# Performance work log

Hardware: AMD Instinct MI355X
Metric: run time of the kernel (lower is better)

The kernel has to match this reference:

```python
import jax, jax.numpy as jnp
import numpy as np

N = 50000      # nodes
E = 640000     # edges
DIN = 256      # in_channels
DE = 64        # edge_dim
H1 = 128       # hidden_channels (conv1 out)
H2 = 64        # hidden_channels//2 (conv2 out)
OUT = 1


def tconv(x, src, dst, edge_attr, Wq, bq, Wk, bk, Wv, bv, We, Ws, bs):
    """PyG TransformerConv, heads=1, concat=True, root_weight=True."""
    n = x.shape[0]
    C = Wq.shape[1]
    q = x @ Wq + bq                      # [N, C]
    k = x @ Wk + bk                      # [N, C]
    v = x @ Wv + bv                      # [N, C]
    e = edge_attr @ We                   # [E, C] (lin_edge has no bias)
    k_e = k[src] + e                     # key_j + edge_emb per edge
    alpha = jnp.sum(q[dst] * k_e, axis=-1) / jnp.sqrt(jnp.float32(C))  # [E]
    # neighborhood softmax over incoming edges of each dst node
    m = jax.ops.segment_max(alpha, dst, num_segments=n)
    ex = jnp.exp(alpha - m[dst])
    denom = jax.ops.segment_sum(ex, dst, num_segments=n)
    a = ex / (denom[dst] + 1e-16)
    msg = a[:, None] * (v[src] + e)      # [E, C]
    out = jax.ops.segment_sum(msg, dst, num_segments=n)  # [N, C]
    return out + x @ Ws + bs             # root/skip connection


def setup_inputs() -> dict:
    key = jax.random.key(0)
    ks = jax.random.split(key, 24)
    p = lambda k, shape: jax.random.normal(k, shape, jnp.float32) * 0.02
    inp = {
        "x": jax.random.normal(ks[0], (N, DIN), jnp.float32),
        "edge_index": jax.random.randint(ks[1], (2, E), 0, N),
        "edge_attr": jax.random.normal(ks[2], (E, DE), jnp.float32),
        # conv1 params (in=DIN -> out=H1)
        "Wq1": p(ks[3], (DIN, H1)), "bq1": jnp.zeros((H1,), jnp.float32),
        "Wk1": p(ks[4], (DIN, H1)), "bk1": jnp.zeros((H1,), jnp.float32),
        "Wv1": p(ks[5], (DIN, H1)), "bv1": jnp.zeros((H1,), jnp.float32),
        "We1": p(ks[6], (DE, H1)),
        "Ws1": p(ks[7], (DIN, H1)), "bs1": jnp.zeros((H1,), jnp.float32),
        # conv2 params (in=H1 -> out=H2)
        "Wq2": p(ks[8], (H1, H2)), "bq2": jnp.zeros((H2,), jnp.float32),
        "Wk2": p(ks[9], (H1, H2)), "bk2": jnp.zeros((H2,), jnp.float32),
        "Wv2": p(ks[10], (H1, H2)), "bv2": jnp.zeros((H2,), jnp.float32),
        "We2": p(ks[11], (DE, H2)),
        "Ws2": p(ks[12], (H1, H2)), "bs2": jnp.zeros((H2,), jnp.float32),
        # classifier
        "Wc": p(ks[13], (H2, OUT)), "bc": jnp.zeros((OUT,), jnp.float32),
    }
    return inp


def reference(x, edge_index, edge_attr,
              Wq1, bq1, Wk1, bk1, Wv1, bv1, We1, Ws1, bs1,
              Wq2, bq2, Wk2, bk2, Wv2, bv2, We2, Ws2, bs2,
              Wc, bc):
    src, dst = edge_index[0], edge_index[1]
    h = tconv(x, src, dst, edge_attr, Wq1, bq1, Wk1, bk1, Wv1, bv1, We1, Ws1, bs1)
    h = jax.nn.relu(h)  # dropout is identity in eval mode
    h = tconv(h, src, dst, edge_attr, Wq2, bq2, Wk2, bk2, Wv2, bv2, We2, Ws2, bs2)
    h = jax.nn.relu(h)
    return h @ Wc + bc  # [N, 1] logits
```

## Files before the change

### kernel.cpp

```cpp
#include <hip/hip_runtime.h>
#include <math.h>

constexpr int NN  = 50000;
constexpr int NE  = 640000;
constexpr int DIN = 256;
constexpr int DE  = 64;
constexpr int H1  = 128;
constexpr int H2  = 64;
constexpr int EWS = H1 + H2;

using u16 = unsigned short;
typedef __attribute__((ext_vector_type(8))) short bf16x8;
typedef __attribute__((ext_vector_type(4))) float f32x4;

__device__ inline u16 f2bf(float f) {
  unsigned u = __float_as_uint(f);
  unsigned r = (u + 0x7FFFu + ((u >> 16) & 1u)) >> 16;
  return (u16)r;
}
__device__ inline float bf2f(u16 h) { return __uint_as_float(((unsigned)h) << 16); }
__device__ inline unsigned pack2(u16 a, u16 b) {
  return (unsigned)a | ((unsigned)b << 16);
}
__device__ inline f32x4 mfma16(bf16x8 a, bf16x8 b, f32x4 c) {
  return __builtin_amdgcn_mfma_f32_16x16x32_bf16(a, b, c, 0, 0, 0);
}

__global__ __launch_bounds__(256) void packwt_kernel(
    const float* __restrict__ W0, const float* __restrict__ W1,
    const float* __restrict__ W2, const float* __restrict__ W3,
    const float* __restrict__ b0, const float* __restrict__ b1,
    const float* __restrict__ b2, const float* __restrict__ b3,
    u16* __restrict__ Bth, u16* __restrict__ Btl, float* __restrict__ bcat,
    int K, int C, int nmats) {
  int total = nmats * C * K;
  for (int idx = blockIdx.x * blockDim.x + threadIdx.x; idx < total;
       idx += gridDim.x * blockDim.x) {
    int k = idx % K;
    int n = idx / K;
    int which = n / C, cc = n % C;
    const float* W = which == 0 ? W0 : which == 1 ? W1 : which == 2 ? W2 : W3;
    float v = W[k * C + cc];
    u16 h = f2bf(v);
    Bth[(size_t)n * K + k] = h;
    Btl[(size_t)n * K + k] = f2bf(v - bf2f(h));
    if (k == 0 && bcat) {
      const float* b = which == 0 ? b0 : which == 1 ? b1 : which == 2 ? b2 : b3;
      bcat[n] = b ? b[cc] : 0.f;
    }
  }
}

__global__ __launch_bounds__(256) void hist_kernel(const int* __restrict__ dst,
                                                   int* __restrict__ deg, int nE) {
  int e = blockIdx.x * blockDim.x + threadIdx.x;
  if (e < nE) atomicAdd(&deg[dst[e]], 1);
}

__global__ __launch_bounds__(256) void scan1_kernel(const int* __restrict__ deg,
                                                    int* __restrict__ part,
                                                    int* __restrict__ chunkSums,
                                                    int n) {
  __shared__ int s[256];
  int tid = threadIdx.x;
  int i = blockIdx.x * 256 + tid;
  int v0 = (i < n) ? deg[i] : 0;
  s[tid] = v0;
  __syncthreads();
  for (int off = 1; off < 256; off <<= 1) {
    int v = (tid >= off) ? s[tid - off] : 0;
    __syncthreads();
    s[tid] += v;
    __syncthreads();
  }
  if (i < n) part[i] = s[tid];
  if (tid == 255) chunkSums[blockIdx.x] = s[255];
}

__global__ __launch_bounds__(256) void scan2_kernel(int* __restrict__ chunkSums,
                                                    int nchunks) {
  __shared__ int s[256];
  int tid = threadIdx.x;
  s[tid] = (tid < nchunks) ? chunkSums[tid] : 0;
  __syncthreads();
  for (int off = 1; off < 256; off <<= 1) {
    int v = (tid >= off) ? s[tid - off] : 0;
    __syncthreads();
    s[tid] += v;
    __syncthreads();
  }
  if (tid < nchunks) chunkSums[tid] = s[tid];
}

__global__ __launch_bounds__(256) void scan3_kernel(const int* __restrict__ deg,
                                                    const int* __restrict__ part,
                                                    const int* __restrict__ chunkSums,
                                                    int* __restrict__ row_start,
                                                    int n, int nE) {
  int i = blockIdx.x * 256 + threadIdx.x;
  if (i < n)
    row_start[i] = part[i] - deg[i] + (blockIdx.x ? chunkSums[blockIdx.x - 1] : 0);
  if (i == 0) row_start[n] = nE;
}

__global__ __launch_bounds__(256) void scatter_kernel(const int* __restrict__ dst,
                                                      const int* __restrict__ row_start,
                                                      int* __restrict__ cursor,
                                                      int* __restrict__ eid, int nE) {
  int e = blockIdx.x * blockDim.x + threadIdx.x;
  if (e >= nE) return;
  int d = dst[e];
  int pos = row_start[d] + atomicAdd(&cursor[d], 1);
  eid[pos] = e;
}

__global__ __launch_bounds__(256) void sort_extract_kernel(
    int* __restrict__ eid, const int* __restrict__ row_start,
    const int* __restrict__ srcI, int* __restrict__ src_csr, int n) {
  int v = blockIdx.x * blockDim.x + threadIdx.x;
  if (v >= n) return;
  int b = row_start[v], e = row_start[v + 1];
  for (int i = b + 1; i < e; i++) {
    int key = eid[i];
    int j = i - 1;
    while (j >= b && eid[j] > key) { eid[j + 1] = eid[j]; j--; }
    eid[j + 1] = key;
  }
  for (int i = b; i < e; i++) src_csr[i] = srcI[eid[i]];
}

template <int BN, int EPI>
__global__ __launch_bounds__(256) void mfma_gemm_kernel(
    const float* __restrict__ A, const int* __restrict__ ridx,
    const u16* __restrict__ Bth, const u16* __restrict__ Btl,
    const float* __restrict__ bias, float* __restrict__ Cout,
    float* __restrict__ Qp, u16* __restrict__ KVp, float* __restrict__ Sp,
    int M, int Nn, int K, int Cl) {
  constexpr int BM = 128, BK = 32;
  constexpr int NI = BN / 32;
  constexpr int SM_STAGE = (BM + BN) * BK * 2;
  constexpr int SM_EPI = (EPI >= 1) ? BM * BN : 0;
  constexpr int SM = SM_STAGE > SM_EPI ? SM_STAGE : SM_EPI;
  __shared__ __align__(16) u16 smem[SM];
  u16* Ah = smem;
  u16* Al = smem + BM * BK;
  u16* Bh = smem + 2 * BM * BK;
  u16* Bl = smem + 2 * BM * BK + BN * BK;
  int tid = threadIdx.x;
  int lane = tid & 63, wid = tid >> 6;
  int wm = wid >> 1, wn = wid & 1;
  int row0 = blockIdx.y * BM, col0 = blockIdx.x * BN;
  int k8 = lane >> 4, rb = lane & 15;

  f32x4 acc[4][NI];
#pragma unroll
  for (int mi = 0; mi < 4; mi++)
#pragma unroll
    for (int ni = 0; ni < NI; ni++) acc[mi][ni] = (f32x4){0.f, 0.f, 0.f, 0.f};

  size_t aoff[2];
  int sdst[2];
  for (int p = 0; p < 2; p++) {
    int idx = p * 256 + tid;
    int r = idx >> 2, c = idx & 3;
    int ar = row0 + r;
    if (ar >= M) ar = M - 1;
    if (ridx) ar = ridx[ar];
    aoff[p] = (size_t)ar * K + c * 8;
    sdst[p] = r * BK + ((c ^ ((r >> 1) & 3)) << 3);
  }

  for (int k0 = 0; k0 < K; k0 += BK) {
    __syncthreads();
#pragma unroll
    for (int p = 0; p < 2; p++) {
      const float* s = A + aoff[p] + k0;
      float4 u = *(const float4*)s, v = *(const float4*)(s + 4);
      float f[8] = {u.x, u.y, u.z, u.w, v.x, v.y, v.z, v.w};
      u16 h[8], l[8];
#pragma unroll
      for (int j = 0; j < 8; j++) {
        h[j] = f2bf(f[j]);
        l[j] = f2bf(f[j] - bf2f(h[j]));
      }
      *(uint4*)&Ah[sdst[p]] = make_uint4(pack2(h[0], h[1]), pack2(h[2], h[3]),
                                         pack2(h[4], h[5]), pack2(h[6], h[7]));
      *(uint4*)&Al[sdst[p]] = make_uint4(pack2(l[0], l[1]), pack2(l[2], l[3]),
                                         pack2(l[4], l[5]), pack2(l[6], l[7]));
    }
#pragma unroll
    for (int p = 0; p < (BN * 4) / 256; p++) {
      int idx = p * 256 + tid;
      int n = idx >> 2, c = idx & 3;
      size_t goff = (size_t)(col0 + n) * K + k0 + c * 8;
      int doff = n * BK + ((c ^ ((n >> 1) & 3)) << 3);
      *(uint4*)&Bh[doff] = *(const uint4*)&Bth[goff];
      *(uint4*)&Bl[doff] = *(const uint4*)&Btl[goff];
    }
    __syncthreads();
    bf16x8 ah[4], al[4], bh[NI], bl[NI];
#pragma unroll
    for (int mi = 0; mi < 4; mi++) {
      int row = wm * 64 + mi * 16 + rb;
      int off = row * BK + ((k8 ^ ((row >> 1) & 3)) << 3);
      ah[mi] = *(const bf16x8*)&Ah[off];
      al[mi] = *(const bf16x8*)&Al[off];
    }
#pragma unroll
    for (int ni = 0; ni < NI; ni++) {
      int cn = wn * (BN / 2) + ni * 16 + rb;
      int off = cn * BK + ((k8 ^ ((cn >> 1) & 3)) << 3);
      bh[ni] = *(const bf16x8*)&Bh[off];
      bl[ni] = *(const bf16x8*)&Bl[off];
    }
#pragma unroll
    for (int mi = 0; mi < 4; mi++)
#pragma unroll
      for (int ni = 0; ni < NI; ni++) {
        f32x4 c = acc[mi][ni];
        c = mfma16(ah[mi], bh[ni], c);
        c = mfma16(al[mi], bh[ni], c);
        c = mfma16(ah[mi], bl[ni], c);
        acc[mi][ni] = c;
      }
  }

  bool kvseg = false;
  if constexpr (EPI == 2) {
    int seg = col0 / Cl;
    kvseg = (seg == 1 || seg == 2);
    if (!kvseg) {
      float* dst = (seg == 0) ? Qp : Sp;
      int cbase = (seg == 0) ? col0 : col0 - 3 * Cl;
#pragma unroll
      for (int ni = 0; ni < NI; ni++) {
        int cfrag = wn * (BN / 2) + ni * 16 + rb;
        float bv = bias ? bias[col0 + cfrag] : 0.f;
#pragma unroll
        for (int mi = 0; mi < 4; mi++) {
#pragma unroll
          for (int q = 0; q < 4; q++) {
            int row = row0 + wm * 64 + mi * 16 + k8 * 4 + q;
            if (row < M)
              dst[(size_t)row * Cl + cbase + cfrag] = acc[mi][ni][q] + bv;
          }
        }
      }
      return;
    }
  }
  if (kvseg) {
    __syncthreads();
    u16* S = smem;
#pragma unroll
    for (int ni = 0; ni < NI; ni++) {
      int coll = wn * (BN / 2) + ni * 16 + rb;
      float bv = bias ? bias[col0 + coll] : 0.f;
#pragma unroll
      for (int mi = 0; mi < 4; mi++) {
#pragma unroll
        for (int q = 0; q < 4; q++) {
          int rowl = wm * 64 + mi * 16 + k8 * 4 + q;
          S[rowl * BN + (coll ^ (((rowl >> 2) & 3) << 4))] =
              f2bf(acc[mi][ni][q] + bv);
        }
      }
    }
    __syncthreads();
    u16* dbase = KVp;
    size_t dstride = 2 * Cl;
    int dcol0 = col0 - Cl;
    constexpr int PASSES = (BM * BN * 2) / (256 * 16);
#pragma unroll
    for (int p = 0; p < PASSES; p++) {
      int idx = p * 256 + tid;
      int r = idx / (BN / 8);
      int cp = idx % (BN / 8);
      int row = row0 + r;
      int cps = cp ^ (((r >> 2) & 3) << 1);
      if (row < M)
        *(uint4*)&dbase[(size_t)row * dstride + dcol0 + cp * 8] =
            *(const uint4*)&S[r * BN + cps * 8];
    }
    return;
  }
  if constexpr (EPI == 0) {
#pragma unroll
    for (int ni = 0; ni < NI; ni++) {
      int col = col0 + wn * (BN / 2) + ni * 16 + rb;
      float bv = bias ? bias[col] : 0.f;
#pragma unroll
      for (int mi = 0; mi < 4; mi++) {
#pragma unroll
        for (int q = 0; q < 4; q++) {
          int row = row0 + wm * 64 + mi * 16 + k8 * 4 + q;
          if (row < M) Cout[(size_t)row * Nn + col] = acc[mi][ni][q] + bv;
        }
      }
    }
  }
}

__global__ __launch_bounds__(512) void edge_gemm_kernel(
    const float* __restrict__ A, const u16* __restrict__ Bth,
    const u16* __restrict__ Btl, u16* __restrict__ Cbf) {
  constexpr int BM = 256, BN = 192, BK = 32, K = DE;
  constexpr int NI = 6;
  __shared__ __align__(16) u16 smem[BM * BK + 2 * BN * BK];
  u16* Ah = smem;
  u16* Bh = smem + BM * BK;
  u16* Bl = smem + BM * BK + BN * BK;
  int tid = threadIdx.x;
  int lane = tid & 63, wid = tid >> 6;
  int wm = wid >> 1, wn = wid & 1;
  int row0 = blockIdx.x * BM;
  int k8 = lane >> 4, rb = lane & 15;

  f32x4 acc[4][NI];
#pragma unroll
  for (int mi = 0; mi < 4; mi++)
#pragma unroll
    for (int ni = 0; ni < NI; ni++) acc[mi][ni] = (f32x4){0.f, 0.f, 0.f, 0.f};

  size_t aoff[2];
  int sdst[2];
#pragma unroll
  for (int p = 0; p < 2; p++) {
    int idx = p * 512 + tid;
    int r = idx >> 2, c = idx & 3;
    aoff[p] = (size_t)(row0 + r) * K + c * 8;
    sdst[p] = r * BK + ((c ^ ((r >> 1) & 3)) << 3);
  }

  for (int k0 = 0; k0 < K; k0 += BK) {
    __syncthreads();
#pragma unroll
    for (int p = 0; p < 2; p++) {
      const float* s = A + aoff[p] + k0;
      float4 u = *(const float4*)s, v = *(const float4*)(s + 4);
      float f[8] = {u.x, u.y, u.z, u.w, v.x, v.y, v.z, v.w};
      u16 h[8];
#pragma unroll
      for (int j = 0; j < 8; j++) h[j] = f2bf(f[j]);
      *(uint4*)&Ah[sdst[p]] = make_uint4(pack2(h[0], h[1]), pack2(h[2], h[3]),
                                         pack2(h[4], h[5]), pack2(h[6], h[7]));
    }
#pragma unroll
    for (int p = 0; p < 2; p++) {
      int idx = p * 512 + tid;
      if (idx < BN * 4) {
        int n = idx >> 2, c = idx & 3;
        size_t goff = (size_t)n * K + k0 + c * 8;
        int doff = n * BK + ((c ^ ((n >> 1) & 3)) << 3);
        *(uint4*)&Bh[doff] = *(const uint4*)&Bth[goff];
        *(uint4*)&Bl[doff] = *(const uint4*)&Btl[goff];
      }
    }
    __syncthreads();
    bf16x8 ah[4], bh[NI], bl[NI];
#pragma unroll
    for (int mi = 0; mi < 4; mi++) {
      int row = wm * 64 + mi * 16 + rb;
      int off = row * BK + ((k8 ^ ((row >> 1) & 3)) << 3);
      ah[mi] = *(const bf16x8*)&Ah[off];
    }
#pragma unroll
    for (int ni = 0; ni < NI; ni++) {
      int cn = wn * 96 + ni * 16 + rb;
      int off = cn * BK + ((k8 ^ ((cn >> 1) & 3)) << 3);
      bh[ni] = *(const bf16x8*)&Bh[off];
      bl[ni] = *(const bf16x8*)&Bl[off];
    }
#pragma unroll
    for (int mi = 0; mi < 4; mi++)
#pragma unroll
      for (int ni = 0; ni < NI; ni++) {
        f32x4 c = acc[mi][ni];
        c = mfma16(ah[mi], bh[ni], c);
        c = mfma16(ah[mi], bl[ni], c);
        acc[mi][ni] = c;
      }
  }

  u16* S = smem;
#pragma unroll
  for (int qtr = 0; qtr < 4; qtr++) {
    __syncthreads();
    if (wm == qtr) {
#pragma unroll
      for (int ni = 0; ni < NI; ni++) {
        int coll = wn * 96 + ni * 16 + rb;
#pragma unroll
        for (int mi = 0; mi < 4; mi++) {
#pragma unroll
          for (int q = 0; q < 4; q++) {
            int rowl = mi * 16 + k8 * 4 + q;
            S[rowl * BN + (coll ^ (((rowl >> 2) & 3) << 4))] =
                f2bf(acc[mi][ni][q]);
          }
        }
      }
    }
    __syncthreads();
#pragma unroll
    for (int p = 0; p < 3; p++) {
      int idx = p * 512 + tid;
      int r = idx / (BN / 8);
      int cp = idx % (BN / 8);
      int row = row0 + qtr * 64 + r;
      int cps = cp ^ (((r >> 2) & 3) << 1);
      *(uint4*)&Cbf[(size_t)row * BN + cp * 8] = *(const uint4*)&S[r * BN + cps * 8];
    }
  }
}

template <int C, int EOFF>
__global__ __launch_bounds__(256) void fused_edge_kernel(
    const float* __restrict__ Q, const float* __restrict__ SKIP,
    const u16* __restrict__ KV, const u16* __restrict__ Ew,
    const int* __restrict__ row_start, const int* __restrict__ src_csr,
    const int* __restrict__ eid, float* __restrict__ h, float scale, int n) {
  constexpr int CPL = C / 64;
  int node = blockIdx.x * 4 + (threadIdx.x >> 6);
  int lane = threadIdx.x & 63;
  if (node >= n) return;
  int ch = lane * CPL;
  float q[CPL], acc[CPL], skip[CPL];
#pragma unroll
  for (int j = 0; j < CPL; j++) {
    q[j] = Q[(size_t)node * C + ch + j];
    skip[j] = SKIP[(size_t)node * C + ch + j];
    acc[j] = 0.f;
  }
  float m = -INFINITY, denom = 0.f;
  int b = row_start[node], e = row_start[node + 1];
  for (int i = b; i < e; i += 4) {
    float part[4], vv[4][CPL];
#pragma unroll
    for (int u = 0; u < 4; u++) {
      int idx = (i + u < e) ? i + u : e - 1;
      int s = src_csr[idx];
      int eo = eid[idx];
      const u16* kvp = KV + (size_t)s * (2 * C);
      const u16* Ee = Ew + (size_t)eo * EWS + EOFF;
      float kk[CPL], ev[CPL];
      if constexpr (CPL == 2) {
        unsigned uk = *(const unsigned*)(kvp + ch);
        unsigned uv = *(const unsigned*)(kvp + C + ch);
        unsigned ue = *(const unsigned*)(Ee + ch);
        kk[0] = bf2f((u16)uk); kk[1] = bf2f((u16)(uk >> 16));
        vv[u][0] = bf2f((u16)uv); vv[u][1] = bf2f((u16)(uv >> 16));
        ev[0] = bf2f((u16)ue); ev[1] = bf2f((u16)(ue >> 16));
      } else {
        kk[0] = bf2f(kvp[ch]);
        vv[u][0] = bf2f(kvp[C + ch]);
        ev[0] = bf2f(Ee[ch]);
      }
      float p = 0.f;
#pragma unroll
      for (int j = 0; j < CPL; j++) {
        p = fmaf(q[j], kk[j] + ev[j], p);
        vv[u][j] += ev[j];
      }
      part[u] = p;
    }
#pragma unroll
    for (int off = 32; off > 0; off >>= 1) {
      part[0] += __shfl_xor(part[0], off);
      part[1] += __shfl_xor(part[1], off);
      part[2] += __shfl_xor(part[2], off);
      part[3] += __shfl_xor(part[3], off);
    }
    float l[4];
#pragma unroll
    for (int u = 0; u < 4; u++)
      l[u] = (i + u < e) ? part[u] * scale : -INFINITY;
    float nm = fmaxf(fmaxf(fmaxf(l[0], l[1]), fmaxf(l[2], l[3])), m);
    float f = expf(m - nm);
    float w[4];
#pragma unroll
    for (int u = 0; u < 4; u++) w[u] = expf(l[u] - nm);
    denom = denom * f + (w[0] + w[1]) + (w[2] + w[3]);
#pragma unroll
    for (int j = 0; j < CPL; j++) {
      float a = acc[j] * f;
      a = fmaf(w[0], vv[0][j], a);
      a = fmaf(w[1], vv[1][j], a);
      a = fmaf(w[2], vv[2][j], a);
      a = fmaf(w[3], vv[3][j], a);
      acc[j] = a;
    }
    m = nm;
  }
  float inv = 1.f / (denom + 1e-16f);
#pragma unroll
  for (int j = 0; j < CPL; j++)
    h[(size_t)node * C + ch + j] = fmaxf(acc[j] * inv + skip[j], 0.f);
}

__global__ __launch_bounds__(256) void classifier_kernel(
    const float* __restrict__ h2, const float* __restrict__ Wc,
    const float* __restrict__ bc, float* __restrict__ out, int n) {
  int w = blockIdx.x * 4 + (threadIdx.x >> 6);
  int lane = threadIdx.x & 63;
  if (w >= n) return;
  float v = h2[(size_t)w * 64 + lane] * Wc[lane];
#pragma unroll
  for (int off = 32; off > 0; off >>= 1) v += __shfl_xor(v, off);
  if (lane == 0) out[w] = v + bc[0];
}

extern "C" void kernel_launch(void* const* d_in, const int* in_sizes, int n_in,
                              void* d_out, int out_size, void* d_ws,
                              size_t ws_size, hipStream_t stream) {
  const float* x         = (const float*)d_in[0];
  const int*   ei        = (const int*)d_in[1];
  const float* edge_attr = (const float*)d_in[2];
  const float* Wq1 = (const float*)d_in[3];  const float* bq1 = (const float*)d_in[4];
  const float* Wk1 = (const float*)d_in[5];  const float* bk1 = (const float*)d_in[6];
  const float* Wv1 = (const float*)d_in[7];  const float* bv1 = (const float*)d_in[8];
  const float* We1 = (const float*)d_in[9];
  const float* Ws1 = (const float*)d_in[10]; const float* bs1 = (const float*)d_in[11];
  const float* Wq2 = (const float*)d_in[12]; const float* bq2 = (const float*)d_in[13];
  const float* Wk2 = (const float*)d_in[14]; const float* bk2 = (const float*)d_in[15];
  const float* Wv2 = (const float*)d_in[16]; const float* bv2 = (const float*)d_in[17];
  const float* We2 = (const float*)d_in[18];
  const float* Ws2 = (const float*)d_in[19]; const float* bs2 = (const float*)d_in[20];
  const float* Wc  = (const float*)d_in[21]; const float* bc  = (const float*)d_in[22];
  float* out = (float*)d_out;

  const int* srcI = ei;
  const int* dstI = ei + NE;

  char* ws = (char*)d_ws;
  size_t off = 0;
  auto alloc = [&](size_t bytes) {
    void* p = ws + off;
    off += (bytes + 255) & ~(size_t)255;
    return p;
  };
  u16*   EwB  = (u16*)alloc((size_t)NE * EWS * 2);
  float* Q1   = (float*)alloc((size_t)NN * H1 * 4);
  float* S1   = (float*)alloc((size_t)NN * H1 * 4);
  u16*   KV1  = (u16*)alloc((size_t)NN * 2 * H1 * 2);
  float* Q2   = (float*)alloc((size_t)NN * H2 * 4);
  float* S2   = (float*)alloc((size_t)NN * H2 * 4);
  u16*   KV2  = (u16*)alloc((size_t)NN * 2 * H2 * 2);
  float* h1   = (float*)alloc((size_t)NN * H1 * 4);
  float* h2   = (float*)alloc((size_t)NN * H2 * 4);
  u16* B1h = (u16*)alloc((size_t)4 * H1 * DIN * 2);
  u16* B1l = (u16*)alloc((size_t)4 * H1 * DIN * 2);
  u16* B2h = (u16*)alloc((size_t)4 * H2 * H1 * 2);
  u16* B2l = (u16*)alloc((size_t)4 * H2 * H1 * 2);
  u16* Ech = (u16*)alloc((size_t)EWS * DE * 2);
  u16* Ecl = (u16*)alloc((size_t)EWS * DE * 2);
  float* b1cat = (float*)alloc(4 * H1 * 4);
  float* b2cat = (float*)alloc(4 * H2 * 4);
  int* deg       = (int*)alloc(NN * 4);
  int* cursor    = (int*)alloc(NN * 4);
  int* row_start = (int*)alloc((NN + 1) * 4);
  int* part      = (int*)alloc(((NN + 255) / 256) * 256 * 4);
  int* chunkSums = (int*)alloc(256 * 4);
  int* eid       = (int*)alloc(NE * 4);
  int* src_csr   = (int*)alloc(NE * 4);
  (void)ws_size; (void)in_sizes; (void)n_in; (void)out_size;

  const int nchunks = (NN + 255) / 256;

  packwt_kernel<<<256, 256, 0, stream>>>(Wq1, Wk1, Wv1, Ws1, bq1, bk1, bv1, bs1,
                                         B1h, B1l, b1cat, DIN, H1, 4);
  packwt_kernel<<<128, 256, 0, stream>>>(Wq2, Wk2, Wv2, Ws2, bq2, bk2, bv2, bs2,
                                         B2h, B2l, b2cat, H1, H2, 4);
  packwt_kernel<<<64, 256, 0, stream>>>(We1, nullptr, nullptr, nullptr, nullptr,
                                        nullptr, nullptr, nullptr, Ech, Ecl,
                                        nullptr, DE, H1, 1);
  packwt_kernel<<<32, 256, 0, stream>>>(We2, nullptr, nullptr, nullptr, nullptr,
                                        nullptr, nullptr, nullptr,
                                        Ech + (size_t)H1 * DE, Ecl + (size_t)H1 * DE,
                                        nullptr, DE, H2, 1);

  hipMemsetAsync(deg, 0, NN * sizeof(int), stream);
  hipMemsetAsync(cursor, 0, NN * sizeof(int), stream);
  hist_kernel<<<(NE + 255) / 256, 256, 0, stream>>>(dstI, deg, NE);
  scan1_kernel<<<nchunks, 256, 0, stream>>>(deg, part, chunkSums, NN);
  scan2_kernel<<<1, 256, 0, stream>>>(chunkSums, nchunks);
  scan3_kernel<<<nchunks, 256, 0, stream>>>(deg, part, chunkSums, row_start, NN, NE);
  scatter_kernel<<<(NE + 255) / 256, 256, 0, stream>>>(dstI, row_start, cursor,
                                                       eid, NE);
  sort_extract_kernel<<<(NN + 255) / 256, 256, 0, stream>>>(eid, row_start, srcI,
                                                            src_csr, NN);

  edge_gemm_kernel<<<NE / 256, 512, 0, stream>>>(edge_attr, Ech, Ecl, EwB);

  mfma_gemm_kernel<128, 2><<<dim3(4 * H1 / 128, (NN + 127) / 128), 256, 0, stream>>>(
      x, nullptr, B1h, B1l, b1cat, nullptr, Q1, KV1, S1, NN, 4 * H1, DIN, H1);
  fused_edge_kernel<H1, 0><<<(NN + 3) / 4, 256, 0, stream>>>(
      Q1, S1, KV1, EwB, row_start, src_csr, eid, h1, 0.08838834764831845f, NN);

  mfma_gemm_kernel<64, 2><<<dim3(4 * H2 / 64, (NN + 127) / 128), 256, 0, stream>>>(
      h1, nullptr, B2h, B2l, b2cat, nullptr, Q2, KV2, S2, NN, 4 * H2, H1, H2);
  fused_edge_kernel<H2, H1><<<(NN + 3) / 4, 256, 0, stream>>>(
      Q2, S2, KV2, EwB, row_start, src_csr, eid, h2, 0.125f, NN);

  classifier_kernel<<<(NN + 3) / 4, 256, 0, stream>>>(h2, Wc, bc, out, NN);
}
```

Measured before the change: 508.6 us.

## Restructure edge GEMM: preload full B tile, direct A register loads, smaller M tile

```diff
diff --git a/kernel.cpp b/kernel.cpp
--- a/kernel.cpp
+++ b/kernel.cpp
@@ -12,6 +12,7 @@
 using u16 = unsigned short;
 typedef __attribute__((ext_vector_type(8))) short bf16x8;
 typedef __attribute__((ext_vector_type(4))) float f32x4;
+typedef __attribute__((ext_vector_type(4))) unsigned int u32x4;
 
 __device__ inline u16 f2bf(float f) {
   unsigned u = __float_as_uint(f);
@@ -301,100 +302,76 @@
   }
 }
 
-__global__ __launch_bounds__(512) void edge_gemm_kernel(
+__global__ __launch_bounds__(512, 4) void edge_gemm_kernel(
     const float* __restrict__ A, const u16* __restrict__ Bth,
     const u16* __restrict__ Btl, u16* __restrict__ Cbf) {
-  constexpr int BM = 256, BN = 192, BK = 32, K = DE;
+  constexpr int BM = 128, BN = 192, K = DE;
   constexpr int NI = 6;
-  __shared__ __align__(16) u16 smem[BM * BK + 2 * BN * BK];
-  u16* Ah = smem;
-  u16* Bh = smem + BM * BK;
-  u16* Bl = smem + BM * BK + BN * BK;
+  __shared__ __align__(16) u16 smem[2 * BN * K];
+  u16* BhL = smem;
+  u16* BlL = smem + BN * K;
   int tid = threadIdx.x;
   int lane = tid & 63, wid = tid >> 6;
   int wm = wid >> 1, wn = wid & 1;
   int row0 = blockIdx.x * BM;
   int k8 = lane >> 4, rb = lane & 15;
 
-  f32x4 acc[4][NI];
-#pragma unroll
-  for (int mi = 0; mi < 4; mi++)
+#pragma unroll
+  for (int p = 0; p < 6; p++) {
+    int idx = p * 512 + tid;
+    bool hi = idx < 1536;
+    int m = hi ? idx : idx - 1536;
+    int n = m >> 3, c = m & 7;
+    const u16* src = (hi ? Bth : Btl) + n * K + c * 8;
+    u16* dst = (hi ? BhL : BlL) + n * K + ((c ^ (n & 7)) << 3);
+    *(uint4*)dst = *(const uint4*)src;
+  }
+  __syncthreads();
+
+  f32x4 acc[2][NI];
+#pragma unroll
+  for (int mi = 0; mi < 2; mi++)
 #pragma unroll
     for (int ni = 0; ni < NI; ni++) acc[mi][ni] = (f32x4){0.f, 0.f, 0.f, 0.f};
 
-  size_t aoff[2];
-  int sdst[2];
-#pragma unroll
-  for (int p = 0; p < 2; p++) {
-    int idx = p * 512 + tid;
-    int r = idx >> 2, c = idx & 3;
-    aoff[p] = (size_t)(row0 + r) * K + c * 8;
-    sdst[p] = r * BK + ((c ^ ((r >> 1) & 3)) << 3);
-  }
-
-  for (int k0 = 0; k0 < K; k0 += BK) {
-    __syncthreads();
-#pragma unroll
-    for (int p = 0; p < 2; p++) {
-      const float* s = A + aoff[p] + k0;
+#pragma unroll
+  for (int k0 = 0; k0 < K; k0 += 32) {
+#pragma unroll
+    for (int mi = 0; mi < 2; mi++) {
+      int row = row0 + wm * 32 + mi * 16 + rb;
+      const float* s = A + (size_t)row * K + k0 + k8 * 8;
       float4 u = *(const float4*)s, v = *(const float4*)(s + 4);
-      float f[8] = {u.x, u.y, u.z, u.w, v.x, v.y, v.z, v.w};
-      u16 h[8];
-#pragma unroll
-      for (int j = 0; j < 8; j++) h[j] = f2bf(f[j]);
-      *(uint4*)&Ah[sdst[p]] = make_uint4(pack2(h[0], h[1]), pack2(h[2], h[3]),
-                                         pack2(h[4], h[5]), pack2(h[6], h[7]));
-    }
-#pragma unroll
-    for (int p = 0; p < 2; p++) {
-      int idx = p * 512 + tid;
-      if (idx < BN * 4) {
-        int n = idx >> 2, c = idx & 3;
-        size_t goff = (size_t)n * K + k0 + c * 8;
-        int doff = n * BK + ((c ^ ((n >> 1) & 3)) << 3);
-        *(uint4*)&Bh[doff] = *(const uint4*)&Bth[goff];
-        *(uint4*)&Bl[doff] = *(const uint4*)&Btl[goff];
-      }
-    }
-    __syncthreads();
-    bf16x8 ah[4], bh[NI], bl[NI];
-#pragma unroll
-    for (int mi = 0; mi < 4; mi++) {
-      int row = wm * 64 + mi * 16 + rb;
-      int off = row * BK + ((k8 ^ ((row >> 1) & 3)) << 3);
-      ah[mi] = *(const bf16x8*)&Ah[off];
-    }
-#pragma unroll
-    for (int ni = 0; ni < NI; ni++) {
-      int cn = wn * 96 + ni * 16 + rb;
-      int off = cn * BK + ((k8 ^ ((cn >> 1) & 3)) << 3);
-      bh[ni] = *(const bf16x8*)&Bh[off];
-      bl[ni] = *(const bf16x8*)&Bl[off];
-    }
-#pragma unroll
-    for (int mi = 0; mi < 4; mi++)
+      uint4 pk = make_uint4(pack2(f2bf(u.x), f2bf(u.y)), pack2(f2bf(u.z), f2bf(u.w)),
+                            pack2(f2bf(v.x), f2bf(v.y)), pack2(f2bf(v.z), f2bf(v.w)));
+      bf16x8 ah = *(bf16x8*)&pk;
+      int chunk = (k0 >> 3) + k8;
 #pragma unroll
       for (int ni = 0; ni < NI; ni++) {
+        int cn = wn * 96 + ni * 16 + rb;
+        int off = cn * K + ((chunk ^ (cn & 7)) << 3);
+        bf16x8 bhf = *(const bf16x8*)&BhL[off];
+        bf16x8 blf = *(const bf16x8*)&BlL[off];
         f32x4 c = acc[mi][ni];
-        c = mfma16(ah[mi], bh[ni], c);
-        c = mfma16(ah[mi], bl[ni], c);
+        c = mfma16(ah, bhf, c);
+        c = mfma16(ah, blf, c);
         acc[mi][ni] = c;
       }
+    }
   }
 
   u16* S = smem;
 #pragma unroll
-  for (int qtr = 0; qtr < 4; qtr++) {
-    __syncthreads();
-    if (wm == qtr) {
+  for (int half = 0; half < 2; half++) {
+    __syncthreads();
+    if ((wm >> 1) == half) {
 #pragma unroll
       for (int ni = 0; ni < NI; ni++) {
         int coll = wn * 96 + ni * 16 + rb;
 #pragma unroll
-        for (int mi = 0; mi < 4; mi++) {
+        for (int mi = 0; mi < 2; mi++) {
 #pragma unroll
           for (int q = 0; q < 4; q++) {
-            int rowl = mi * 16 + k8 * 4 + q;
+            int rowl = (wm & 1) * 32 + mi * 16 + k8 * 4 + q;
             S[rowl * BN + (coll ^ (((rowl >> 2) & 3) << 4))] =
                 f2bf(acc[mi][ni][q]);
           }
@@ -407,9 +384,10 @@
       int idx = p * 512 + tid;
       int r = idx / (BN / 8);
       int cp = idx % (BN / 8);
-      int row = row0 + qtr * 64 + r;
+      int row = row0 + half * 64 + r;
       int cps = cp ^ (((r >> 2) & 3) << 1);
-      *(uint4*)&Cbf[(size_t)row * BN + cp * 8] = *(const uint4*)&S[r * BN + cps * 8];
+      __builtin_nontemporal_store(*(const u32x4*)&S[r * BN + cps * 8],
+                                  (u32x4*)&Cbf[(size_t)row * BN + cp * 8]);
     }
   }
 }
@@ -590,7 +568,7 @@
   sort_extract_kernel<<<(NN + 255) / 256, 256, 0, stream>>>(eid, row_start, srcI,
                                                             src_csr, NN);
 
-  edge_gemm_kernel<<<NE / 256, 512, 0, stream>>>(edge_attr, Ech, Ecl, EwB);
+  edge_gemm_kernel<<<NE / 128, 512, 0, stream>>>(edge_attr, Ech, Ecl, EwB);
 
   mfma_gemm_kernel<128, 2><<<dim3(4 * H1 / 128, (NN + 127) / 128), 256, 0, stream>>>(
       x, nullptr, B1h, B1l, b1cat, nullptr, Q1, KV1, S1, NN, 4 * H1, DIN, H1);
```

Result: faster. 488.4 us (-4.0%).
